# Kernel tuning notes

Measured on AMD Instinct MI355X. Metric: run time of the kernel, lower is better.

The kernel has to match this reference:

```python
import jax, jax.numpy as jnp
import numpy as np

BATCH = 16
N_NODES_TOT = 131072  # batch * 8192
N_EDGES_TOT = 262144  # batch * 16384
D = 128


def _mlp(x, W1, b1, W2, b2):
    return jax.nn.relu(x @ W1 + b1) @ W2 + b2


def setup_inputs() -> dict:
    key = jax.random.key(0)
    ks = jax.random.split(key, 16)
    s = lambda fan_in: 1.0 / np.sqrt(fan_in)
    return {
        "nodes": jax.random.normal(ks[0], (N_NODES_TOT, D), jnp.float32),
        "edges": jax.random.normal(ks[1], (N_EDGES_TOT, D), jnp.float32),
        "global_latent": jax.random.normal(ks[2], (BATCH, D), jnp.float32),
        "eW1": jax.random.normal(ks[3], (4 * D, D), jnp.float32) * s(4 * D),
        "eb1": jnp.zeros((D,), jnp.float32),
        "eW2": jax.random.normal(ks[4], (D, D), jnp.float32) * s(D),
        "eb2": jnp.zeros((D,), jnp.float32),
        "nW1": jax.random.normal(ks[5], (3 * D, D), jnp.float32) * s(3 * D),
        "nb1": jnp.zeros((D,), jnp.float32),
        "nW2": jax.random.normal(ks[6], (D, D), jnp.float32) * s(D),
        "nb2": jnp.zeros((D,), jnp.float32),
        "gW1": jax.random.normal(ks[7], (3 * D, D), jnp.float32) * s(3 * D),
        "gb1": jnp.zeros((D,), jnp.float32),
        "gW2": jax.random.normal(ks[8], (D, D), jnp.float32) * s(D),
        "gb2": jnp.zeros((D,), jnp.float32),
        "rn_w": jnp.full((1,), -5.0, jnp.float32),  # softplus resnet-multiplier init
        "receivers": jax.random.randint(ks[9], (N_EDGES_TOT,), 0, N_NODES_TOT, jnp.int32),
        "senders": jax.random.randint(ks[10], (N_EDGES_TOT,), 0, N_NODES_TOT, jnp.int32),
        "node_graph_idx": jnp.sort(jax.random.randint(ks[11], (N_NODES_TOT,), 0, BATCH, jnp.int32)),
        "edge_graph_idx": jnp.sort(jax.random.randint(ks[12], (N_EDGES_TOT,), 0, BATCH, jnp.int32)),
    }


def reference(nodes, edges, global_latent,
              eW1, eb1, eW2, eb2,
              nW1, nb1, nW2, nb2,
              gW1, gb1, gW2, gb2,
              rn_w,
              receivers, senders, node_graph_idx, edge_graph_idx):
    n_nodes_tot = nodes.shape[0]
    batch = global_latent.shape[0]

    # ---- edge block: gather -> concat -> MLP ----
    sent = nodes[senders]                       # [E, D]
    recv = nodes[receivers]                     # [E, D]
    g_edge = global_latent[edge_graph_idx]      # [E, D]
    edges_update = _mlp(jnp.concatenate([edges, sent, recv, g_edge], axis=1),
                        eW1, eb1, eW2, eb2)     # [E, D]

    # ---- node block: segment_sum of edges onto receivers ----
    adjacent = jax.ops.segment_sum(edges_update, receivers, num_segments=n_nodes_tot)
    g_node = global_latent[node_graph_idx]
    nodes_update = _mlp(jnp.concatenate([nodes, adjacent, g_node], axis=1),
                        nW1, nb1, nW2, nb2)     # [N, D]

    # ---- global block: per-graph aggregates ----
    node_agg = jax.ops.segment_sum(nodes_update, node_graph_idx, num_segments=batch)
    edge_agg = jax.ops.segment_sum(edges_update, edge_graph_idx, num_segments=batch)
    global_update = _mlp(jnp.concatenate([node_agg, edge_agg, global_latent], axis=1),
                         gW1, gb1, gW2, gb2)    # [B, D]

    # ---- residual with softplus multiplier (dropout off / inference) ----
    m = jax.nn.softplus(rn_w)
    return (nodes + m * nodes_update,
            edges + m * edges_update,
            global_latent + m * global_update)
```

## Files before the change

kernel.cpp:

```cpp
#include <hip/hip_runtime.h>
#include <hip/hip_bf16.h>

#define N_NODES 131072
#define N_EDGES 262144
#define NBATCH  16

typedef __attribute__((ext_vector_type(8))) __bf16 bf16x8;
typedef __attribute__((ext_vector_type(4))) float  fx4;

__device__ __forceinline__ fx4 mfma16(bf16x8 a, bf16x8 b, fx4 c) {
    return __builtin_amdgcn_mfma_f32_16x16x32_bf16(a, b, c, 0, 0, 0);
}

__device__ __forceinline__ bf16x8 load_row8(const float* p) {
    const fx4* q = (const fx4*)p;
    fx4 a = q[0], b = q[1];
    bf16x8 r;
    r[0] = (__bf16)a[0]; r[1] = (__bf16)a[1]; r[2] = (__bf16)a[2]; r[3] = (__bf16)a[3];
    r[4] = (__bf16)b[0]; r[5] = (__bf16)b[1]; r[6] = (__bf16)b[2]; r[7] = (__bf16)b[3];
    return r;
}

__global__ void gn_swizzle(const float* __restrict__ src, __bf16* __restrict__ dst, int KS)
{
    int idx = blockIdx.x * 256 + threadIdx.x;
    int total = KS * 32 * 128;
    if (idx >= total) return;
    int j    = idx & 7;
    int lane = (idx >> 3) & 63;
    int rem  = idx >> 9;
    int ks   = rem % KS;
    int t    = rem / KS;
    int n = t * 16 + (lane & 15);
    int k = ks * 32 + ((lane >> 4) << 3) + j;
    dst[idx] = (__bf16)src[k * 128 + n];
}

__global__ __launch_bounds__(256) void gn_edge_kernel(
    const float* __restrict__ nodes, const float* __restrict__ edges,
    const float* __restrict__ gl,
    const __bf16* __restrict__ W1sw, const float* __restrict__ b1,
    const __bf16* __restrict__ W2sw, const float* __restrict__ b2,
    const float* __restrict__ rn_w,
    const int* __restrict__ senders, const int* __restrict__ receivers,
    const int* __restrict__ egid,
    float* __restrict__ out_edges,
    float* __restrict__ adjacent,
    float* __restrict__ edge_agg)
{
    __shared__ int s_send[128], s_recv[128], s_gid[128];
    __shared__ __align__(16) __bf16 s_H[4][32][152];
    __shared__ float s_agg[NBATCH * 128];

    const int tid  = threadIdx.x;
    const int wave = tid >> 6, lane = tid & 63;
    const int m = lane & 15, q = lane >> 4;
    const int eblock = blockIdx.x * 128;

    if (tid < 128) {
        int e = eblock + tid;
        s_send[tid] = senders[e];
        s_recv[tid] = receivers[e];
        s_gid[tid]  = egid[e];
    }
    for (int i = tid; i < NBATCH * 128; i += 256) s_agg[i] = 0.f;
    __syncthreads();

    const int wbase = wave * 32;

    const float* aptr[2][4];
    #pragma unroll
    for (int rt = 0; rt < 2; ++rt) {
        int er = wbase + rt * 16 + m;
        size_t eg = (size_t)(eblock + er);
        aptr[rt][0] = edges + eg * 128;
        aptr[rt][1] = nodes + (size_t)s_send[er] * 128;
        aptr[rt][2] = nodes + (size_t)s_recv[er] * 128;
        aptr[rt][3] = gl    + (size_t)s_gid[er]  * 128;
    }

    fx4 acc[2][8];
    #pragma unroll
    for (int rt = 0; rt < 2; ++rt)
        #pragma unroll
        for (int t = 0; t < 8; ++t) acc[rt][t] = fx4{0.f, 0.f, 0.f, 0.f};

    const bf16x8* W1v = (const bf16x8*)W1sw;
    #pragma unroll
    for (int ks = 0; ks < 16; ++ks) {
        const int seg  = ks >> 2;
        const int koff = ((ks & 3) << 5) + (q << 3);
        bf16x8 a0 = load_row8(aptr[0][seg] + koff);
        bf16x8 a1 = load_row8(aptr[1][seg] + koff);
        #pragma unroll
        for (int t = 0; t < 8; ++t) {
            bf16x8 b = W1v[(t * 16 + ks) * 64 + lane];
            acc[0][t] = mfma16(a0, b, acc[0][t]);
            acc[1][t] = mfma16(a1, b, acc[1][t]);
        }
    }

    #pragma unroll
    for (int t = 0; t < 8; ++t) {
        float bv = b1[t * 16 + m];
        #pragma unroll
        for (int rt = 0; rt < 2; ++rt)
            #pragma unroll
            for (int r = 0; r < 4; ++r) {
                float h = acc[rt][t][r] + bv;
                s_H[wave][rt * 16 + q * 4 + r][t * 16 + m] = (__bf16)fmaxf(h, 0.f);
            }
    }
    __syncthreads();

    #pragma unroll
    for (int rt = 0; rt < 2; ++rt)
        #pragma unroll
        for (int t = 0; t < 8; ++t) acc[rt][t] = fx4{0.f, 0.f, 0.f, 0.f};

    const bf16x8* W2v = (const bf16x8*)W2sw;
    #pragma unroll
    for (int ks = 0; ks < 4; ++ks) {
        bf16x8 a0 = *(const bf16x8*)&s_H[wave][m][ks * 32 + q * 8];
        bf16x8 a1 = *(const bf16x8*)&s_H[wave][16 + m][ks * 32 + q * 8];
        #pragma unroll
        for (int t = 0; t < 8; ++t) {
            bf16x8 b = W2v[(t * 4 + ks) * 64 + lane];
            acc[0][t] = mfma16(a0, b, acc[0][t]);
            acc[1][t] = mfma16(a1, b, acc[1][t]);
        }
    }

    const float mres = log1pf(expf(rn_w[0]));

    #pragma unroll
    for (int rt = 0; rt < 2; ++rt) {
        int er0 = wbase + rt * 16 + q * 4;
        bool sameg = (s_gid[er0] == s_gid[er0 + 3]);
        #pragma unroll
        for (int t = 0; t < 8; ++t) {
            int col = t * 16 + m;
            float bv = b2[col];
            float usum = 0.f;
            #pragma unroll
            for (int r = 0; r < 4; ++r) {
                int er = er0 + r;
                size_t eg = (size_t)(eblock + er);
                float u = acc[rt][t][r] + bv;
                out_edges[eg * 128 + col] = edges[eg * 128 + col] + mres * u;
                unsafeAtomicAdd(&adjacent[(size_t)s_recv[er] * 128 + col], u);
                if (sameg) usum += u;
                else       atomicAdd(&s_agg[s_gid[er] * 128 + col], u);
            }
            if (sameg) atomicAdd(&s_agg[s_gid[er0] * 128 + col], usum);
        }
    }
    __syncthreads();
    for (int i = tid; i < NBATCH * 128; i += 256) {
        float v = s_agg[i];
        if (v != 0.f) unsafeAtomicAdd(&edge_agg[i], v);
    }
}

__global__ __launch_bounds__(256) void gn_node_kernel(
    const float* __restrict__ nodes,
    const float* __restrict__ gl,
    const __bf16* __restrict__ W1sw, const float* __restrict__ b1,
    const __bf16* __restrict__ W2sw, const float* __restrict__ b2,
    const float* __restrict__ rn_w,
    const int* __restrict__ ngid,
    const float* __restrict__ adjacent,
    float* __restrict__ out_nodes,
    float* __restrict__ node_agg)
{
    __shared__ int s_gid[128];
    __shared__ __align__(16) __bf16 s_H[4][32][152];
    __shared__ float s_agg[NBATCH * 128];

    const int tid  = threadIdx.x;
    const int wave = tid >> 6, lane = tid & 63;
    const int m = lane & 15, q = lane >> 4;
    const int nblock = blockIdx.x * 128;

    if (tid < 128) s_gid[tid] = ngid[nblock + tid];
    for (int i = tid; i < NBATCH * 128; i += 256) s_agg[i] = 0.f;
    __syncthreads();

    const int wbase = wave * 32;
    const float* ap[2][3];
    #pragma unroll
    for (int rt = 0; rt < 2; ++rt) {
        int vr = wbase + rt * 16 + m;
        size_t vg = (size_t)(nblock + vr);
        ap[rt][0] = nodes + vg * 128;
        ap[rt][1] = adjacent + vg * 128;
        ap[rt][2] = gl + (size_t)s_gid[vr] * 128;
    }

    fx4 acc[2][8];
    #pragma unroll
    for (int rt = 0; rt < 2; ++rt)
        #pragma unroll
        for (int t = 0; t < 8; ++t) acc[rt][t] = fx4{0.f, 0.f, 0.f, 0.f};

    const bf16x8* W1v = (const bf16x8*)W1sw;
    #pragma unroll
    for (int ks = 0; ks < 12; ++ks) {
        const int seg  = ks >> 2;
        const int koff = ((ks & 3) << 5) + (q << 3);
        bf16x8 a0 = load_row8(ap[0][seg] + koff);
        bf16x8 a1 = load_row8(ap[1][seg] + koff);
        #pragma unroll
        for (int t = 0; t < 8; ++t) {
            bf16x8 b = W1v[(t * 12 + ks) * 64 + lane];
            acc[0][t] = mfma16(a0, b, acc[0][t]);
            acc[1][t] = mfma16(a1, b, acc[1][t]);
        }
    }

    #pragma unroll
    for (int t = 0; t < 8; ++t) {
        float bv = b1[t * 16 + m];
        #pragma unroll
        for (int rt = 0; rt < 2; ++rt)
            #pragma unroll
            for (int r = 0; r < 4; ++r) {
                float h = acc[rt][t][r] + bv;
                s_H[wave][rt * 16 + q * 4 + r][t * 16 + m] = (__bf16)fmaxf(h, 0.f);
            }
    }
    __syncthreads();

    #pragma unroll
    for (int rt = 0; rt < 2; ++rt)
        #pragma unroll
        for (int t = 0; t < 8; ++t) acc[rt][t] = fx4{0.f, 0.f, 0.f, 0.f};

    const bf16x8* W2v = (const bf16x8*)W2sw;
    #pragma unroll
    for (int ks = 0; ks < 4; ++ks) {
        bf16x8 a0 = *(const bf16x8*)&s_H[wave][m][ks * 32 + q * 8];
        bf16x8 a1 = *(const bf16x8*)&s_H[wave][16 + m][ks * 32 + q * 8];
        #pragma unroll
        for (int t = 0; t < 8; ++t) {
            bf16x8 b = W2v[(t * 4 + ks) * 64 + lane];
            acc[0][t] = mfma16(a0, b, acc[0][t]);
            acc[1][t] = mfma16(a1, b, acc[1][t]);
        }
    }

    const float mres = log1pf(expf(rn_w[0]));

    #pragma unroll
    for (int rt = 0; rt < 2; ++rt) {
        int vr0 = wbase + rt * 16 + q * 4;
        bool sameg = (s_gid[vr0] == s_gid[vr0 + 3]);
        #pragma unroll
        for (int t = 0; t < 8; ++t) {
            int col = t * 16 + m;
            float bv = b2[col];
            float usum = 0.f;
            #pragma unroll
            for (int r = 0; r < 4; ++r) {
                int vr = vr0 + r;
                size_t vg = (size_t)(nblock + vr);
                float u = acc[rt][t][r] + bv;
                out_nodes[vg * 128 + col] = nodes[vg * 128 + col] + mres * u;
                if (sameg) usum += u;
                else       atomicAdd(&s_agg[s_gid[vr] * 128 + col], u);
            }
            if (sameg) atomicAdd(&s_agg[s_gid[vr0] * 128 + col], usum);
        }
    }
    __syncthreads();
    for (int i = tid; i < NBATCH * 128; i += 256) {
        float v = s_agg[i];
        if (v != 0.f) unsafeAtomicAdd(&node_agg[i], v);
    }
}

__global__ void gn_global_kernel(
    const float* __restrict__ gl,
    const float* __restrict__ gW1, const float* __restrict__ gb1,
    const float* __restrict__ gW2, const float* __restrict__ gb2,
    const float* __restrict__ rn_w,
    const float* __restrict__ node_agg, const float* __restrict__ edge_agg,
    float* __restrict__ out_gl)
{
    __shared__ float s_x[384];
    __shared__ float s_h[128];
    const int row = blockIdx.x, t = threadIdx.x;

    s_x[t]       = node_agg[row * 128 + t];
    s_x[128 + t] = edge_agg[row * 128 + t];
    s_x[256 + t] = gl[row * 128 + t];
    __syncthreads();

    float acc = gb1[t];
    for (int k = 0; k < 384; ++k) acc += s_x[k] * gW1[k * 128 + t];
    s_h[t] = fmaxf(acc, 0.f);
    __syncthreads();

    float acc2 = gb2[t];
    for (int k = 0; k < 128; ++k) acc2 += s_h[k] * gW2[k * 128 + t];
    const float mres = log1pf(expf(rn_w[0]));
    out_gl[row * 128 + t] = gl[row * 128 + t] + mres * acc2;
}

extern "C" void kernel_launch(void* const* d_in, const int* in_sizes, int n_in,
                              void* d_out, int out_size, void* d_ws, size_t ws_size,
                              hipStream_t stream)
{
    const float* nodes = (const float*)d_in[0];
    const float* edges = (const float*)d_in[1];
    const float* gl    = (const float*)d_in[2];
    const float* eW1   = (const float*)d_in[3];
    const float* eb1   = (const float*)d_in[4];
    const float* eW2   = (const float*)d_in[5];
    const float* eb2   = (const float*)d_in[6];
    const float* nW1   = (const float*)d_in[7];
    const float* nb1   = (const float*)d_in[8];
    const float* nW2   = (const float*)d_in[9];
    const float* nb2   = (const float*)d_in[10];
    const float* gW1   = (const float*)d_in[11];
    const float* gb1   = (const float*)d_in[12];
    const float* gW2   = (const float*)d_in[13];
    const float* gb2   = (const float*)d_in[14];
    const float* rn_w  = (const float*)d_in[15];
    const int* receivers = (const int*)d_in[16];
    const int* senders   = (const int*)d_in[17];
    const int* ngid      = (const int*)d_in[18];
    const int* egid      = (const int*)d_in[19];

    char* ws = (char*)d_ws;
    __bf16* eW1sw    = (__bf16*)(ws + 0);
    __bf16* eW2sw    = (__bf16*)(ws + 131072);
    __bf16* nW1sw    = (__bf16*)(ws + 163840);
    __bf16* nW2sw    = (__bf16*)(ws + 262144);
    float*  edge_agg = (float*)(ws + 294912);
    float*  node_agg = (float*)(ws + 303104);
    float*  adjacent = (float*)(ws + 311296);

    float* out_nodes = (float*)d_out;
    float* out_edges = out_nodes + (size_t)N_NODES * 128;
    float* out_gl    = out_edges + (size_t)N_EDGES * 128;

    hipMemsetAsync(ws + 294912, 0, (size_t)16384 + 67108864, stream);

    gn_swizzle<<<dim3(256), dim3(256), 0, stream>>>(eW1, eW1sw, 16);
    gn_swizzle<<<dim3(64),  dim3(256), 0, stream>>>(eW2, eW2sw, 4);
    gn_swizzle<<<dim3(192), dim3(256), 0, stream>>>(nW1, nW1sw, 12);
    gn_swizzle<<<dim3(64),  dim3(256), 0, stream>>>(nW2, nW2sw, 4);

    gn_edge_kernel<<<dim3(N_EDGES / 128), dim3(256), 0, stream>>>(
        nodes, edges, gl, eW1sw, eb1, eW2sw, eb2, rn_w,
        senders, receivers, egid, out_edges, adjacent, edge_agg);

    gn_node_kernel<<<dim3(N_NODES / 128), dim3(256), 0, stream>>>(
        nodes, gl, nW1sw, nb1, nW2sw, nb2, rn_w,
        ngid, adjacent, out_nodes, node_agg);

    gn_global_kernel<<<dim3(NBATCH), dim3(128), 0, stream>>>(
        gl, gW1, gb1, gW2, gb2, rn_w, node_agg, edge_agg, out_gl);
}
```

Measured before the change: 852.9 us.

## Cut register and LDS footprint of edge/node MLP kernels for higher occupancy

Each wave now processes its 32 rows as two sequential 16-row passes instead of holding two accumulator tiles, which halves accumulator registers. Shared memory shrinks by dropping the index staging arrays and limiting the per-block aggregate buffer to 4 graphs relative to the block's first graph id, with a global-atomic fallback for the rest. Launch bounds request 6 blocks per CU, and the input loads are double-buffered two k-steps ahead. In exchange, every W1/W2 fragment is reloaded once per pass, which doubles weight traffic, and indices are read from global memory rather than LDS.

```diff
diff --git a/kernel.cpp b/kernel.cpp
--- a/kernel.cpp
+++ b/kernel.cpp
@@ -12,9 +12,11 @@
     return __builtin_amdgcn_mfma_f32_16x16x32_bf16(a, b, c, 0, 0, 0);
 }
 
-__device__ __forceinline__ bf16x8 load_row8(const float* p) {
+__device__ __forceinline__ void ld8(const float* p, fx4& x, fx4& y) {
     const fx4* q = (const fx4*)p;
-    fx4 a = q[0], b = q[1];
+    x = q[0]; y = q[1];
+}
+__device__ __forceinline__ bf16x8 cvt8(fx4 a, fx4 b) {
     bf16x8 r;
     r[0] = (__bf16)a[0]; r[1] = (__bf16)a[1]; r[2] = (__bf16)a[2]; r[3] = (__bf16)a[3];
     r[4] = (__bf16)b[0]; r[5] = (__bf16)b[1]; r[6] = (__bf16)b[2]; r[7] = (__bf16)b[3];
@@ -36,7 +38,7 @@
     dst[idx] = (__bf16)src[k * 128 + n];
 }
 
-__global__ __launch_bounds__(256) void gn_edge_kernel(
+__global__ __launch_bounds__(256, 6) void gn_edge_kernel(
     const float* __restrict__ nodes, const float* __restrict__ edges,
     const float* __restrict__ gl,
     const __bf16* __restrict__ W1sw, const float* __restrict__ b1,
@@ -48,121 +50,115 @@
     float* __restrict__ adjacent,
     float* __restrict__ edge_agg)
 {
-    __shared__ int s_send[128], s_recv[128], s_gid[128];
-    __shared__ __align__(16) __bf16 s_H[4][32][152];
-    __shared__ float s_agg[NBATCH * 128];
+    __shared__ __align__(16) __bf16 s_H[4][16][136];
+    __shared__ float s_agg[4 * 128];
 
     const int tid  = threadIdx.x;
     const int wave = tid >> 6, lane = tid & 63;
     const int m = lane & 15, q = lane >> 4;
+    const int qo = q << 3;
     const int eblock = blockIdx.x * 128;
-
-    if (tid < 128) {
-        int e = eblock + tid;
-        s_send[tid] = senders[e];
-        s_recv[tid] = receivers[e];
-        s_gid[tid]  = egid[e];
+    const int wbase  = wave * 32;
+    const int g0 = egid[eblock];
+
+    for (int i = tid; i < 4 * 128; i += 256) s_agg[i] = 0.f;
+    __syncthreads();
+
+    const bf16x8* W1v = (const bf16x8*)W1sw;
+    const bf16x8* W2v = (const bf16x8*)W2sw;
+    const float mres = log1pf(expf(rn_w[0]));
+
+    #pragma unroll 1
+    for (int p = 0; p < 2; ++p) {
+        const int e = eblock + wbase + p * 16 + m;
+        const float* aseg[4];
+        aseg[0] = edges + (size_t)e * 128;
+        aseg[1] = nodes + (size_t)senders[e]   * 128;
+        aseg[2] = nodes + (size_t)receivers[e] * 128;
+        aseg[3] = gl    + (size_t)egid[e]      * 128;
+
+        fx4 acc[8];
+        #pragma unroll
+        for (int t = 0; t < 8; ++t) acc[t] = fx4{0.f, 0.f, 0.f, 0.f};
+
+        fx4 buf[2][2];
+        ld8(aseg[0] + qo,      buf[0][0], buf[0][1]);
+        ld8(aseg[0] + 32 + qo, buf[1][0], buf[1][1]);
+        #pragma unroll
+        for (int ks = 0; ks < 16; ++ks) {
+            bf16x8 a = cvt8(buf[ks & 1][0], buf[ks & 1][1]);
+            if (ks < 14) {
+                const int kn = ks + 2;
+                ld8(aseg[kn >> 2] + ((kn & 3) << 5) + qo, buf[ks & 1][0], buf[ks & 1][1]);
+            }
+            #pragma unroll
+            for (int t = 0; t < 8; ++t)
+                acc[t] = mfma16(a, W1v[(t * 16 + ks) * 64 + lane], acc[t]);
+        }
+
+        #pragma unroll
+        for (int t = 0; t < 8; ++t) {
+            float bv = b1[t * 16 + m];
+            #pragma unroll
+            for (int r = 0; r < 4; ++r)
+                s_H[wave][q * 4 + r][t * 16 + m] = (__bf16)fmaxf(acc[t][r] + bv, 0.f);
+        }
+
+        #pragma unroll
+        for (int t = 0; t < 8; ++t) acc[t] = fx4{0.f, 0.f, 0.f, 0.f};
+
+        #pragma unroll
+        for (int ks = 0; ks < 4; ++ks) {
+            bf16x8 a = *(const bf16x8*)&s_H[wave][m][ks * 32 + qo];
+            #pragma unroll
+            for (int t = 0; t < 8; ++t)
+                acc[t] = mfma16(a, W2v[(t * 4 + ks) * 64 + lane], acc[t]);
+        }
+
+        const int er0 = eblock + wbase + p * 16 + q * 4;
+        int rcv[4], gd[4];
+        #pragma unroll
+        for (int r = 0; r < 4; ++r) {
+            rcv[r] = receivers[er0 + r];
+            gd[r]  = egid[er0 + r];
+        }
+        const bool sameg = (gd[0] == gd[3]);
+        const int rel0 = gd[0] - g0;
+
+        #pragma unroll
+        for (int t = 0; t < 8; ++t) {
+            const int col = t * 16 + m;
+            const float bv = b2[col];
+            float usum = 0.f;
+            #pragma unroll
+            for (int r = 0; r < 4; ++r) {
+                const size_t eg = (size_t)(er0 + r);
+                float u = acc[t][r] + bv;
+                out_edges[eg * 128 + col] = edges[eg * 128 + col] + mres * u;
+                unsafeAtomicAdd(&adjacent[(size_t)rcv[r] * 128 + col], u);
+                if (sameg) usum += u;
+                else {
+                    int rel = gd[r] - g0;
+                    if (rel < 4) atomicAdd(&s_agg[rel * 128 + col], u);
+                    else         unsafeAtomicAdd(&edge_agg[gd[r] * 128 + col], u);
+                }
+            }
+            if (sameg) {
+                if (rel0 < 4) atomicAdd(&s_agg[rel0 * 128 + col], usum);
+                else          unsafeAtomicAdd(&edge_agg[gd[0] * 128 + col], usum);
+            }
+        }
     }
-    for (int i = tid; i < NBATCH * 128; i += 256) s_agg[i] = 0.f;
-    __syncthreads();
-
-    const int wbase = wave * 32;
-
-    const float* aptr[2][4];
-    #pragma unroll
-    for (int rt = 0; rt < 2; ++rt) {
-        int er = wbase + rt * 16 + m;
-        size_t eg = (size_t)(eblock + er);
-        aptr[rt][0] = edges + eg * 128;
-        aptr[rt][1] = nodes + (size_t)s_send[er] * 128;
-        aptr[rt][2] = nodes + (size_t)s_recv[er] * 128;
-        aptr[rt][3] = gl    + (size_t)s_gid[er]  * 128;
+
+    __syncthreads();
+    for (int i = tid; i < 4 * 128; i += 256) {
+        float v = s_agg[i];
+        if (v != 0.f)
+            unsafeAtomicAdd(&edge_agg[(g0 + (i >> 7)) * 128 + (i & 127)], v);
     }
-
-    fx4 acc[2][8];
-    #pragma unroll
-    for (int rt = 0; rt < 2; ++rt)
-        #pragma unroll
-        for (int t = 0; t < 8; ++t) acc[rt][t] = fx4{0.f, 0.f, 0.f, 0.f};
-
-    const bf16x8* W1v = (const bf16x8*)W1sw;
-    #pragma unroll
-    for (int ks = 0; ks < 16; ++ks) {
-        const int seg  = ks >> 2;
-        const int koff = ((ks & 3) << 5) + (q << 3);
-        bf16x8 a0 = load_row8(aptr[0][seg] + koff);
-        bf16x8 a1 = load_row8(aptr[1][seg] + koff);
-        #pragma unroll
-        for (int t = 0; t < 8; ++t) {
-            bf16x8 b = W1v[(t * 16 + ks) * 64 + lane];
-            acc[0][t] = mfma16(a0, b, acc[0][t]);
-            acc[1][t] = mfma16(a1, b, acc[1][t]);
-        }
-    }
-
-    #pragma unroll
-    for (int t = 0; t < 8; ++t) {
-        float bv = b1[t * 16 + m];
-        #pragma unroll
-        for (int rt = 0; rt < 2; ++rt)
-            #pragma unroll
-            for (int r = 0; r < 4; ++r) {
-                float h = acc[rt][t][r] + bv;
-                s_H[wave][rt * 16 + q * 4 + r][t * 16 + m] = (__bf16)fmaxf(h, 0.f);
-            }
-    }
-    __syncthreads();
-
-    #pragma unroll
-    for (int rt = 0; rt < 2; ++rt)
-        #pragma unroll
-        for (int t = 0; t < 8; ++t) acc[rt][t] = fx4{0.f, 0.f, 0.f, 0.f};
-
-    const bf16x8* W2v = (const bf16x8*)W2sw;
-    #pragma unroll
-    for (int ks = 0; ks < 4; ++ks) {
-        bf16x8 a0 = *(const bf16x8*)&s_H[wave][m][ks * 32 + q * 8];
-        bf16x8 a1 = *(const bf16x8*)&s_H[wave][16 + m][ks * 32 + q * 8];
-        #pragma unroll
-        for (int t = 0; t < 8; ++t) {
-            bf16x8 b = W2v[(t * 4 + ks) * 64 + lane];
-            acc[0][t] = mfma16(a0, b, acc[0][t]);
-            acc[1][t] = mfma16(a1, b, acc[1][t]);
-        }
-    }
-
-    const float mres = log1pf(expf(rn_w[0]));
-
-    #pragma unroll
-    for (int rt = 0; rt < 2; ++rt) {
-        int er0 = wbase + rt * 16 + q * 4;
-        bool sameg = (s_gid[er0] == s_gid[er0 + 3]);
-        #pragma unroll
-        for (int t = 0; t < 8; ++t) {
-            int col = t * 16 + m;
-            float bv = b2[col];
-            float usum = 0.f;
-            #pragma unroll
-            for (int r = 0; r < 4; ++r) {
-                int er = er0 + r;
-                size_t eg = (size_t)(eblock + er);
-                float u = acc[rt][t][r] + bv;
-                out_edges[eg * 128 + col] = edges[eg * 128 + col] + mres * u;
-                unsafeAtomicAdd(&adjacent[(size_t)s_recv[er] * 128 + col], u);
-                if (sameg) usum += u;
-                else       atomicAdd(&s_agg[s_gid[er] * 128 + col], u);
-            }
-            if (sameg) atomicAdd(&s_agg[s_gid[er0] * 128 + col], usum);
-        }
-    }
-    __syncthreads();
-    for (int i = tid; i < NBATCH * 128; i += 256) {
-        float v = s_agg[i];
-        if (v != 0.f) unsafeAtomicAdd(&edge_agg[i], v);
-    }
-}
-
-__global__ __launch_bounds__(256) void gn_node_kernel(
+}
+
+__global__ __launch_bounds__(256, 6) void gn_node_kernel(
     const float* __restrict__ nodes,
     const float* __restrict__ gl,
     const __bf16* __restrict__ W1sw, const float* __restrict__ b1,
@@ -173,109 +169,106 @@
     float* __restrict__ out_nodes,
     float* __restrict__ node_agg)
 {
-    __shared__ int s_gid[128];
-    __shared__ __align__(16) __bf16 s_H[4][32][152];
-    __shared__ float s_agg[NBATCH * 128];
+    __shared__ __align__(16) __bf16 s_H[4][16][136];
+    __shared__ float s_agg[4 * 128];
 
     const int tid  = threadIdx.x;
     const int wave = tid >> 6, lane = tid & 63;
     const int m = lane & 15, q = lane >> 4;
+    const int qo = q << 3;
     const int nblock = blockIdx.x * 128;
-
-    if (tid < 128) s_gid[tid] = ngid[nblock + tid];
-    for (int i = tid; i < NBATCH * 128; i += 256) s_agg[i] = 0.f;
-    __syncthreads();
-
-    const int wbase = wave * 32;
-    const float* ap[2][3];
-    #pragma unroll
-    for (int rt = 0; rt < 2; ++rt) {
-        int vr = wbase + rt * 16 + m;
-        size_t vg = (size_t)(nblock + vr);
-        ap[rt][0] = nodes + vg * 128;
-        ap[rt][1] = adjacent + vg * 128;
-        ap[rt][2] = gl + (size_t)s_gid[vr] * 128;
-    }
-
-    fx4 acc[2][8];
-    #pragma unroll
-    for (int rt = 0; rt < 2; ++rt)
-        #pragma unroll
-        for (int t = 0; t < 8; ++t) acc[rt][t] = fx4{0.f, 0.f, 0.f, 0.f};
+    const int wbase  = wave * 32;
+    const int g0 = ngid[nblock];
+
+    for (int i = tid; i < 4 * 128; i += 256) s_agg[i] = 0.f;
+    __syncthreads();
 
     const bf16x8* W1v = (const bf16x8*)W1sw;
-    #pragma unroll
-    for (int ks = 0; ks < 12; ++ks) {
-        const int seg  = ks >> 2;
-        const int koff = ((ks & 3) << 5) + (q << 3);
-        bf16x8 a0 = load_row8(ap[0][seg] + koff);
-        bf16x8 a1 = load_row8(ap[1][seg] + koff);
+    const bf16x8* W2v = (const bf16x8*)W2sw;
+    const float mres = log1pf(expf(rn_w[0]));
+
+    #pragma unroll 1
+    for (int p = 0; p < 2; ++p) {
+        const int v = nblock + wbase + p * 16 + m;
+        const float* aseg[3];
+        aseg[0] = nodes    + (size_t)v * 128;
+        aseg[1] = adjacent + (size_t)v * 128;
+        aseg[2] = gl       + (size_t)ngid[v] * 128;
+
+        fx4 acc[8];
+        #pragma unroll
+        for (int t = 0; t < 8; ++t) acc[t] = fx4{0.f, 0.f, 0.f, 0.f};
+
+        fx4 buf[2][2];
+        ld8(aseg[0] + qo,      buf[0][0], buf[0][1]);
+        ld8(aseg[0] + 32 + qo, buf[1][0], buf[1][1]);
+        #pragma unroll
+        for (int ks = 0; ks < 12; ++ks) {
+            bf16x8 a = cvt8(buf[ks & 1][0], buf[ks & 1][1]);
+            if (ks < 10) {
+                const int kn = ks + 2;
+                ld8(aseg[kn >> 2] + ((kn & 3) << 5) + qo, buf[ks & 1][0], buf[ks & 1][1]);
+            }
+            #pragma unroll
+            for (int t = 0; t < 8; ++t)
+                acc[t] = mfma16(a, W1v[(t * 12 + ks) * 64 + lane], acc[t]);
+        }
+
         #pragma unroll
         for (int t = 0; t < 8; ++t) {
-            bf16x8 b = W1v[(t * 12 + ks) * 64 + lane];
-            acc[0][t] = mfma16(a0, b, acc[0][t]);
-            acc[1][t] = mfma16(a1, b, acc[1][t]);
-        }
-    }
-
-    #pragma unroll
-    for (int t = 0; t < 8; ++t) {
-        float bv = b1[t * 16 + m];
-        #pragma unroll
-        for (int rt = 0; rt < 2; ++rt)
+            float bv = b1[t * 16 + m];
+            #pragma unroll
+            for (int r = 0; r < 4; ++r)
+                s_H[wave][q * 4 + r][t * 16 + m] = (__bf16)fmaxf(acc[t][r] + bv, 0.f);
+        }
+
+        #pragma unroll
+        for (int t = 0; t < 8; ++t) acc[t] = fx4{0.f, 0.f, 0.f, 0.f};
+
+        #pragma unroll
+        for (int ks = 0; ks < 4; ++ks) {
+            bf16x8 a = *(const bf16x8*)&s_H[wave][m][ks * 32 + qo];
+            #pragma unroll
+            for (int t = 0; t < 8; ++t)
+                acc[t] = mfma16(a, W2v[(t * 4 + ks) * 64 + lane], acc[t]);
+        }
+
+        const int vr0 = nblock + wbase + p * 16 + q * 4;
+        int gd[4];
+        #pragma unroll
+        for (int r = 0; r < 4; ++r) gd[r] = ngid[vr0 + r];
+        const bool sameg = (gd[0] == gd[3]);
+        const int rel0 = gd[0] - g0;
+
+        #pragma unroll
+        for (int t = 0; t < 8; ++t) {
+            const int col = t * 16 + m;
+            const float bv = b2[col];
+            float usum = 0.f;
             #pragma unroll
             for (int r = 0; r < 4; ++r) {
-                float h = acc[rt][t][r] + bv;
-                s_H[wave][rt * 16 + q * 4 + r][t * 16 + m] = (__bf16)fmaxf(h, 0.f);
-            }
-    }
-    __syncthreads();
-
-    #pragma unroll
-    for (int rt = 0; rt < 2; ++rt)
-        #pragma unroll
-        for (int t = 0; t < 8; ++t) acc[rt][t] = fx4{0.f, 0.f, 0.f, 0.f};
-
-    const bf16x8* W2v = (const bf16x8*)W2sw;
-    #pragma unroll
-    for (int ks = 0; ks < 4; ++ks) {
-        bf16x8 a0 = *(const bf16x8*)&s_H[wave][m][ks * 32 + q * 8];
-        bf16x8 a1 = *(const bf16x8*)&s_H[wave][16 + m][ks * 32 + q * 8];
-        #pragma unroll
-        for (int t = 0; t < 8; ++t) {
-            bf16x8 b = W2v[(t * 4 + ks) * 64 + lane];
-            acc[0][t] = mfma16(a0, b, acc[0][t]);
-            acc[1][t] = mfma16(a1, b, acc[1][t]);
-        }
-    }
-
-    const float mres = log1pf(expf(rn_w[0]));
-
-    #pragma unroll
-    for (int rt = 0; rt < 2; ++rt) {
-        int vr0 = wbase + rt * 16 + q * 4;
-        bool sameg = (s_gid[vr0] == s_gid[vr0 + 3]);
-        #pragma unroll
-        for (int t = 0; t < 8; ++t) {
-            int col = t * 16 + m;
-            float bv = b2[col];
-            float usum = 0.f;
-            #pragma unroll
-            for (int r = 0; r < 4; ++r) {
-                int vr = vr0 + r;
-                size_t vg = (size_t)(nblock + vr);
-                float u = acc[rt][t][r] + bv;
+                const size_t vg = (size_t)(vr0 + r);
+                float u = acc[t][r] + bv;
                 out_nodes[vg * 128 + col] = nodes[vg * 128 + col] + mres * u;
                 if (sameg) usum += u;
-                else       atomicAdd(&s_agg[s_gid[vr] * 128 + col], u);
-            }
-            if (sameg) atomicAdd(&s_agg[s_gid[vr0] * 128 + col], usum);
+                else {
+                    int rel = gd[r] - g0;
+                    if (rel < 4) atomicAdd(&s_agg[rel * 128 + col], u);
+                    else         unsafeAtomicAdd(&node_agg[gd[r] * 128 + col], u);
+                }
+            }
+            if (sameg) {
+                if (rel0 < 4) atomicAdd(&s_agg[rel0 * 128 + col], usum);
+                else          unsafeAtomicAdd(&node_agg[gd[0] * 128 + col], usum);
+            }
         }
     }
-    __syncthreads();
-    for (int i = tid; i < NBATCH * 128; i += 256) {
+
+    __syncthreads();
+    for (int i = tid; i < 4 * 128; i += 256) {
         float v = s_agg[i];
-        if (v != 0.f) unsafeAtomicAdd(&node_agg[i], v);
+        if (v != 0.f)
+            unsafeAtomicAdd(&node_agg[(g0 + (i >> 7)) * 128 + (i & 127)], v);
     }
 }
 
```

New measurement: 2.119 ms. +148.5%, slower.
